# Performance work log

Measured on AMD Instinct MI355X. Metric: run time of the kernel, lower is better.

The kernel has to match this reference:

```python
import jax, jax.numpy as jnp
import numpy as np

NUM_LAYERS = 4
HIDDEN = 32
INPUT = 2
B = 16384
T = 64


def setup_inputs() -> dict:
    key = jax.random.key(0)
    ks = jax.random.split(key, 8)
    s = 1.0 / np.sqrt(HIDDEN)  # PyTorch LSTM default init scale
    return {
        "x": jax.random.normal(ks[0], (B, 3, T), dtype=jnp.float32),
        "W_ih0": jax.random.uniform(ks[1], (4 * HIDDEN, INPUT), minval=-s, maxval=s, dtype=jnp.float32),
        "W_ih": jax.random.uniform(ks[2], (NUM_LAYERS - 1, 4 * HIDDEN, HIDDEN), minval=-s, maxval=s, dtype=jnp.float32),
        "W_hh": jax.random.uniform(ks[3], (NUM_LAYERS, 4 * HIDDEN, HIDDEN), minval=-s, maxval=s, dtype=jnp.float32),
        "b_ih": jax.random.uniform(ks[4], (NUM_LAYERS, 4 * HIDDEN), minval=-s, maxval=s, dtype=jnp.float32),
        "b_hh": jax.random.uniform(ks[5], (NUM_LAYERS, 4 * HIDDEN), minval=-s, maxval=s, dtype=jnp.float32),
        "W_lin": jax.random.uniform(ks[6], (1, HIDDEN), minval=-s, maxval=s, dtype=jnp.float32),
        "b_lin": jax.random.uniform(ks[7], (1,), minval=-s, maxval=s, dtype=jnp.float32),
    }


def _lstm_cell(inp, h, c, Wih, Whh, b):
    # inp: [B, in_dim]; h, c: [B, H]; Wih: [4H, in_dim]; Whh: [4H, H]; b: [4H]
    gates = inp @ Wih.T + h @ Whh.T + b  # [B, 4H]
    i, f, g, o = jnp.split(gates, 4, axis=-1)  # PyTorch gate order: i, f, g, o
    i = jax.nn.sigmoid(i)
    f = jax.nn.sigmoid(f)
    g = jnp.tanh(g)
    o = jax.nn.sigmoid(o)
    c_new = f * c + i * g
    h_new = o * jnp.tanh(c_new)
    return h_new, c_new


def reference(x, W_ih0, W_ih, W_hh, b_ih, b_hh, W_lin, b_lin):
    # x: [B, 3, T]; channel 2 (id) is discarded, as in the original forward.
    feats = x[:, :2, :]                         # [B, 2, T]
    xs = jnp.transpose(feats, (2, 0, 1))        # [T, B, 2]
    bsz = x.shape[0]
    h0 = jnp.zeros((NUM_LAYERS, bsz, HIDDEN), dtype=x.dtype)
    c0 = jnp.zeros((NUM_LAYERS, bsz, HIDDEN), dtype=x.dtype)
    bias = b_ih + b_hh  # [L, 4H]

    def step(carry, xt):
        h, c = carry  # each [L, B, H]
        inp = xt
        hs, cs = [], []
        for l in range(NUM_LAYERS):
            Wih = W_ih0 if l == 0 else W_ih[l - 1]
            h_new, c_new = _lstm_cell(inp, h[l], c[l], Wih, W_hh[l], bias[l])
            hs.append(h_new)
            cs.append(c_new)
            inp = h_new
        return (jnp.stack(hs), jnp.stack(cs)), None

    (h, c), _ = jax.lax.scan(step, (h0, c0), xs)
    # last timestep's top-layer output -> linear -> sigmoid -> squeeze to [B]
    out = jax.nn.sigmoid(h[-1] @ W_lin.T + b_lin)  # [B, 1]
    return out.squeeze(-1)
```

## Files before the change

kernel.cpp:

```cpp
#include <hip/hip_runtime.h>

typedef float  f32x4  __attribute__((ext_vector_type(4)));
typedef short  bf16x8 __attribute__((ext_vector_type(8)));

#define LOG2E    1.4426950408889634f
#define TWOLOG2E 2.8853900817779268f

__device__ __forceinline__ unsigned short f2b(float f) {
    unsigned int u = __builtin_bit_cast(unsigned int, f);
    u += 0x7fffu + ((u >> 16) & 1u);
    return (unsigned short)(u >> 16);
}
__device__ __forceinline__ float b2f(unsigned short s) {
    unsigned int u = ((unsigned int)s) << 16;
    return __builtin_bit_cast(float, u);
}
__device__ __forceinline__ unsigned int pk2(float lo, float hi) {
    return (unsigned int)f2b(lo) | ((unsigned int)f2b(hi) << 16);
}
__device__ __forceinline__ float sig2(float xh) {
    return __builtin_amdgcn_rcpf(1.0f + __builtin_amdgcn_exp2f(-xh));
}
__device__ __forceinline__ float th2(float xh) {
    return 2.0f * __builtin_amdgcn_rcpf(1.0f + __builtin_amdgcn_exp2f(-xh)) - 1.0f;
}
__device__ __forceinline__ float thc(float c) {
    return 2.0f * __builtin_amdgcn_rcpf(1.0f + __builtin_amdgcn_exp2f(c * -TWOLOG2E)) - 1.0f;
}

__global__ __launch_bounds__(256, 4)
void lstm_mfma(const float* __restrict__ xg,  const float* __restrict__ Wih0,
               const float* __restrict__ Wih, const float* __restrict__ Whh,
               const float* __restrict__ bih, const float* __restrict__ bhh,
               const float* __restrict__ Wlin,const float* __restrict__ blin,
               float* __restrict__ out) {
    __shared__ short        hb[4 * 2 * 640] __attribute__((aligned(16)));
    __shared__ unsigned int xb[64 * 16];

    const int tid  = threadIdx.x;
    const int wv   = __builtin_amdgcn_readfirstlane(tid >> 6);
    const int lane = tid & 63;
    const int m    = lane & 15;
    const int q    = lane >> 4;
    const int row0 = blockIdx.x * 16;

    for (int i = tid; i < 2560; i += 256) ((unsigned int*)hb)[i] = 0u;

    for (int i = tid; i < 1024; i += 256) {
        int r = i >> 6, t = i & 63;
        float x0 = xg[(size_t)(row0 + r) * 192 + t];
        float x1 = xg[(size_t)(row0 + r) * 192 + 64 + t];
        xb[t * 16 + r] = pk2(x0, x1);
    }

    bf16x8 bfr[8][2];
    float  bv[8];
#pragma unroll
    for (int g = 0; g < 8; ++g) {
        const int   T    = g >> 1;
        const int   rowG = T * 32 + 2 * m + (g & 1);
        const float sc   = (T == 2) ? TWOLOG2E : LOG2E;
        bv[g] = (bih[wv * 128 + rowG] + bhh[wv * 128 + rowG]) * sc;
#pragma unroll
        for (int c = 0; c < 2; ++c) {
            const int k0 = c * 32 + q * 8;
            float w[8];
            if (wv == 0) {
                if (c == 0) {
#pragma unroll
                    for (int jj = 0; jj < 8; ++jj) w[jj] = 0.0f;
                    if (q == 0) { w[0] = Wih0[rowG * 2]; w[1] = Wih0[rowG * 2 + 1]; }
                } else {
                    const float* src = Whh + rowG * 32 + (k0 - 32);
#pragma unroll
                    for (int jj = 0; jj < 8; ++jj) w[jj] = src[jj];
                }
            } else {
                const float* src = (c == 0) ? (Wih + (wv - 1) * 4096 + rowG * 32 + k0)
                                            : (Whh + wv * 4096 + rowG * 32 + (k0 - 32));
#pragma unroll
                for (int jj = 0; jj < 8; ++jj) w[jj] = src[jj];
            }
            bf16x8 fr;
#pragma unroll
            for (int jj = 0; jj < 8; ++jj) fr[jj] = (short)f2b(w[jj] * sc);
            bfr[g][c] = fr;
        }
    }

    float cst[2][4];
#pragma unroll
    for (int hf = 0; hf < 2; ++hf)
#pragma unroll
        for (int r = 0; r < 4; ++r) cst[hf][r] = 0.0f;

    __syncthreads();

    for (int s = 0; s < 67; ++s) {
        const int t = s - wv;
        if (t >= 0 && t < 64) {
            const int rp = (s + 1) & 1;
            const int wp = s & 1;
            const short* hrin  = hb + ((wv > 0 ? wv - 1 : 0) * 2 + rp) * 640;
            const short* hrrec = hb + (wv * 2 + rp) * 640;
            short*       hw    = hb + (wv * 2 + wp) * 640;

            bf16x8 a0, a1;
            if (wv == 0) {
                unsigned int xd = xb[t * 16 + m];
                unsigned int lo = (q == 0) ? xd : 0u;
                union { unsigned int u[4]; bf16x8 v; } au;
                au.u[0] = lo; au.u[1] = 0u; au.u[2] = 0u; au.u[3] = 0u;
                a0 = au.v;
            } else {
                a0 = *(const bf16x8*)(hrin + m * 40 + q * 8);
            }
            a1 = *(const bf16x8*)(hrrec + m * 40 + q * 8);

            float h0[4];
#pragma unroll
            for (int hf = 0; hf < 2; ++hf) {
                f32x4 zz = {0.f, 0.f, 0.f, 0.f};
                f32x4 ai = __builtin_amdgcn_mfma_f32_16x16x32_bf16(a0, bfr[0 + hf][0], zz, 0, 0, 0);
                ai       = __builtin_amdgcn_mfma_f32_16x16x32_bf16(a1, bfr[0 + hf][1], ai, 0, 0, 0);
                f32x4 af = __builtin_amdgcn_mfma_f32_16x16x32_bf16(a0, bfr[2 + hf][0], zz, 0, 0, 0);
                af       = __builtin_amdgcn_mfma_f32_16x16x32_bf16(a1, bfr[2 + hf][1], af, 0, 0, 0);
                f32x4 ag = __builtin_amdgcn_mfma_f32_16x16x32_bf16(a0, bfr[4 + hf][0], zz, 0, 0, 0);
                ag       = __builtin_amdgcn_mfma_f32_16x16x32_bf16(a1, bfr[4 + hf][1], ag, 0, 0, 0);
                f32x4 ao = __builtin_amdgcn_mfma_f32_16x16x32_bf16(a0, bfr[6 + hf][0], zz, 0, 0, 0);
                ao       = __builtin_amdgcn_mfma_f32_16x16x32_bf16(a1, bfr[6 + hf][1], ao, 0, 0, 0);
#pragma unroll
                for (int r = 0; r < 4; ++r) {
                    float i_ = sig2(ai[r] + bv[0 + hf]);
                    float f_ = sig2(af[r] + bv[2 + hf]);
                    float g_ = th2 (ag[r] + bv[4 + hf]);
                    float o_ = sig2(ao[r] + bv[6 + hf]);
                    float cn = f_ * cst[hf][r] + i_ * g_;
                    cst[hf][r] = cn;
                    float hh = o_ * thc(cn);
                    if (hf == 0) {
                        h0[r] = hh;
                    } else {
                        ((unsigned int*)hw)[(q * 4 + r) * 20 + m] = pk2(h0[r], hh);
                    }
                }
            }
        }
        __syncthreads();
    }

    if (tid < 16) {
        const short* h3 = hb + (3 * 2 + 0) * 640;
        float s = blin[0];
#pragma unroll
        for (int k = 0; k < 32; ++k)
            s += Wlin[k] * b2f((unsigned short)h3[tid * 40 + k]);
        out[row0 + tid] = sig2(s * LOG2E);
    }
}

extern "C" void kernel_launch(void* const* d_in, const int* in_sizes, int n_in,
                              void* d_out, int out_size, void* d_ws, size_t ws_size,
                              hipStream_t stream) {
    const float* x    = (const float*)d_in[0];
    const float* Wih0 = (const float*)d_in[1];
    const float* Wih  = (const float*)d_in[2];
    const float* Whh  = (const float*)d_in[3];
    const float* bih  = (const float*)d_in[4];
    const float* bhh  = (const float*)d_in[5];
    const float* Wlin = (const float*)d_in[6];
    const float* blin = (const float*)d_in[7];
    float* out = (float*)d_out;

    lstm_mfma<<<1024, 256, 0, stream>>>(x, Wih0, Wih, Whh, bih, bhh, Wlin, blin, out);
}
```

Baseline: 261.7 us.

## Process two row tiles and two timesteps per sync with fused gate math

Each block now handles 32 batch rows as two 16-row tiles, and each wavefront advances two timesteps per barrier using a deeper double-buffered LDS layout, which halves the number of __syncthreads in the layer-wavefront pipeline. The bias is folded into the MFMA accumulator init and pre-negated scaling is applied to weights. The gate math is restructured to share reciprocals (sigmoid·tanh combined into one rcp). The costs are fewer blocks, higher register pressure and more LDS (launch bounds drop to 2 blocks/CU), and intra-wave dependency between the two timesteps.

```diff
diff --git a/kernel.cpp b/kernel.cpp
--- a/kernel.cpp
+++ b/kernel.cpp
@@ -3,8 +3,9 @@
 typedef float  f32x4  __attribute__((ext_vector_type(4)));
 typedef short  bf16x8 __attribute__((ext_vector_type(8)));
 
-#define LOG2E    1.4426950408889634f
-#define TWOLOG2E 2.8853900817779268f
+#define LOG2E      1.4426950408889634f
+#define NLOG2E    -1.4426950408889634f
+#define NTWOLOG2E -2.8853900817779268f
 
 __device__ __forceinline__ unsigned short f2b(float f) {
     unsigned int u = __builtin_bit_cast(unsigned int, f);
@@ -18,39 +19,32 @@
 __device__ __forceinline__ unsigned int pk2(float lo, float hi) {
     return (unsigned int)f2b(lo) | ((unsigned int)f2b(hi) << 16);
 }
-__device__ __forceinline__ float sig2(float xh) {
-    return __builtin_amdgcn_rcpf(1.0f + __builtin_amdgcn_exp2f(-xh));
-}
-__device__ __forceinline__ float th2(float xh) {
-    return 2.0f * __builtin_amdgcn_rcpf(1.0f + __builtin_amdgcn_exp2f(-xh)) - 1.0f;
-}
-__device__ __forceinline__ float thc(float c) {
-    return 2.0f * __builtin_amdgcn_rcpf(1.0f + __builtin_amdgcn_exp2f(c * -TWOLOG2E)) - 1.0f;
-}
+__device__ __forceinline__ float frcp(float x) { return __builtin_amdgcn_rcpf(x); }
+__device__ __forceinline__ float fex2(float x) { return __builtin_amdgcn_exp2f(x); }
 
-__global__ __launch_bounds__(256, 4)
+__global__ __launch_bounds__(256, 2)
 void lstm_mfma(const float* __restrict__ xg,  const float* __restrict__ Wih0,
                const float* __restrict__ Wih, const float* __restrict__ Whh,
                const float* __restrict__ bih, const float* __restrict__ bhh,
                const float* __restrict__ Wlin,const float* __restrict__ blin,
                float* __restrict__ out) {
-    __shared__ short        hb[4 * 2 * 640] __attribute__((aligned(16)));
-    __shared__ unsigned int xb[64 * 16];
+    __shared__ short        hb[16 * 1280] __attribute__((aligned(16)));
+    __shared__ unsigned int xb[64 * 32];
 
     const int tid  = threadIdx.x;
     const int wv   = __builtin_amdgcn_readfirstlane(tid >> 6);
     const int lane = tid & 63;
     const int m    = lane & 15;
     const int q    = lane >> 4;
-    const int row0 = blockIdx.x * 16;
+    const int row0 = blockIdx.x * 32;
 
-    for (int i = tid; i < 2560; i += 256) ((unsigned int*)hb)[i] = 0u;
+    for (int i = tid; i < 10240; i += 256) ((unsigned int*)hb)[i] = 0u;
 
-    for (int i = tid; i < 1024; i += 256) {
+    for (int i = tid; i < 2048; i += 256) {
         int r = i >> 6, t = i & 63;
         float x0 = xg[(size_t)(row0 + r) * 192 + t];
         float x1 = xg[(size_t)(row0 + r) * 192 + 64 + t];
-        xb[t * 16 + r] = pk2(x0, x1);
+        xb[t * 32 + r] = pk2(x0, x1);
     }
 
     bf16x8 bfr[8][2];
@@ -59,7 +53,7 @@
     for (int g = 0; g < 8; ++g) {
         const int   T    = g >> 1;
         const int   rowG = T * 32 + 2 * m + (g & 1);
-        const float sc   = (T == 2) ? TWOLOG2E : LOG2E;
+        const float sc   = (T == 2) ? NTWOLOG2E : NLOG2E;
         bv[g] = (bih[wv * 128 + rowG] + bhh[wv * 128 + rowG]) * sc;
 #pragma unroll
         for (int c = 0; c < 2; ++c) {
@@ -88,74 +82,87 @@
         }
     }
 
-    float cst[2][4];
+    float cst[2][2][4];
 #pragma unroll
-    for (int hf = 0; hf < 2; ++hf)
+    for (int tt = 0; tt < 2; ++tt)
 #pragma unroll
-        for (int r = 0; r < 4; ++r) cst[hf][r] = 0.0f;
+        for (int hf = 0; hf < 2; ++hf)
+#pragma unroll
+            for (int r = 0; r < 4; ++r) cst[tt][hf][r] = 0.0f;
 
     __syncthreads();
 
-    for (int s = 0; s < 67; ++s) {
-        const int t = s - wv;
-        if (t >= 0 && t < 64) {
-            const int rp = (s + 1) & 1;
-            const int wp = s & 1;
-            const short* hrin  = hb + ((wv > 0 ? wv - 1 : 0) * 2 + rp) * 640;
-            const short* hrrec = hb + (wv * 2 + rp) * 640;
-            short*       hw    = hb + (wv * 2 + wp) * 640;
-
+    auto cell_step = [&](int t, const short* pa0, const short* pa1, short* hwr) {
+#pragma unroll
+        for (int tt = 0; tt < 2; ++tt) {
             bf16x8 a0, a1;
             if (wv == 0) {
-                unsigned int xd = xb[t * 16 + m];
-                unsigned int lo = (q == 0) ? xd : 0u;
+                unsigned int xd = xb[t * 32 + tt * 16 + m];
                 union { unsigned int u[4]; bf16x8 v; } au;
-                au.u[0] = lo; au.u[1] = 0u; au.u[2] = 0u; au.u[3] = 0u;
+                au.u[0] = (q == 0) ? xd : 0u; au.u[1] = 0u; au.u[2] = 0u; au.u[3] = 0u;
                 a0 = au.v;
             } else {
-                a0 = *(const bf16x8*)(hrin + m * 40 + q * 8);
+                a0 = *(const bf16x8*)(pa0 + (tt * 16 + m) * 40 + q * 8);
             }
-            a1 = *(const bf16x8*)(hrrec + m * 40 + q * 8);
+            a1 = *(const bf16x8*)(pa1 + (tt * 16 + m) * 40 + q * 8);
 
+            f32x4 acc[8];
+#pragma unroll
+            for (int g = 0; g < 8; ++g) {
+                f32x4 cb = {bv[g], bv[g], bv[g], bv[g]};
+                acc[g] = __builtin_amdgcn_mfma_f32_16x16x32_bf16(a0, bfr[g][0], cb, 0, 0, 0);
+                acc[g] = __builtin_amdgcn_mfma_f32_16x16x32_bf16(a1, bfr[g][1], acc[g], 0, 0, 0);
+            }
             float h0[4];
 #pragma unroll
             for (int hf = 0; hf < 2; ++hf) {
-                f32x4 zz = {0.f, 0.f, 0.f, 0.f};
-                f32x4 ai = __builtin_amdgcn_mfma_f32_16x16x32_bf16(a0, bfr[0 + hf][0], zz, 0, 0, 0);
-                ai       = __builtin_amdgcn_mfma_f32_16x16x32_bf16(a1, bfr[0 + hf][1], ai, 0, 0, 0);
-                f32x4 af = __builtin_amdgcn_mfma_f32_16x16x32_bf16(a0, bfr[2 + hf][0], zz, 0, 0, 0);
-                af       = __builtin_amdgcn_mfma_f32_16x16x32_bf16(a1, bfr[2 + hf][1], af, 0, 0, 0);
-                f32x4 ag = __builtin_amdgcn_mfma_f32_16x16x32_bf16(a0, bfr[4 + hf][0], zz, 0, 0, 0);
-                ag       = __builtin_amdgcn_mfma_f32_16x16x32_bf16(a1, bfr[4 + hf][1], ag, 0, 0, 0);
-                f32x4 ao = __builtin_amdgcn_mfma_f32_16x16x32_bf16(a0, bfr[6 + hf][0], zz, 0, 0, 0);
-                ao       = __builtin_amdgcn_mfma_f32_16x16x32_bf16(a1, bfr[6 + hf][1], ao, 0, 0, 0);
 #pragma unroll
                 for (int r = 0; r < 4; ++r) {
-                    float i_ = sig2(ai[r] + bv[0 + hf]);
-                    float f_ = sig2(af[r] + bv[2 + hf]);
-                    float g_ = th2 (ag[r] + bv[4 + hf]);
-                    float o_ = sig2(ao[r] + bv[6 + hf]);
-                    float cn = f_ * cst[hf][r] + i_ * g_;
-                    cst[hf][r] = cn;
-                    float hh = o_ * thc(cn);
+                    float ei = fex2(acc[0 + hf][r]);
+                    float ef = fex2(acc[2 + hf][r]);
+                    float eg = fex2(acc[4 + hf][r]);
+                    float eo = fex2(acc[6 + hf][r]);
+                    float ig = (1.0f - eg) * frcp((1.0f + ei) * (1.0f + eg));
+                    float fc = cst[tt][hf][r] * frcp(1.0f + ef);
+                    float cn = ig + fc;
+                    cst[tt][hf][r] = cn;
+                    float ec = fex2(cn * NTWOLOG2E);
+                    float hh = (1.0f - ec) * frcp((1.0f + eo) * (1.0f + ec));
                     if (hf == 0) {
                         h0[r] = hh;
                     } else {
-                        ((unsigned int*)hw)[(q * 4 + r) * 20 + m] = pk2(h0[r], hh);
+                        ((unsigned int*)hwr)[(tt * 16 + q * 4 + r) * 20 + m] = pk2(h0[r], hh);
                     }
                 }
             }
         }
+    };
+
+    for (int S = 0; S < 35; ++S) {
+        const int t0 = 2 * (S - wv);
+        if (t0 >= 0 && t0 <= 62) {
+            const int p  = S & 1;
+            const int pb = p ^ 1;
+            short*       Lc0 = hb + ((wv * 2 + p ) * 2    ) * 1280;
+            short*       Lc1 = Lc0 + 1280;
+            const short* Lp1 = hb + ((wv * 2 + pb) * 2 + 1) * 1280;
+            const int    lb  = (wv > 0) ? (wv - 1) : 0;
+            const short* Dp0 = hb + ((lb * 2 + pb) * 2    ) * 1280;
+            const short* Dp1 = Dp0 + 1280;
+
+            cell_step(t0,     Dp0, Lp1, Lc0);
+            cell_step(t0 + 1, Dp1, Lc0, Lc1);
+        }
         __syncthreads();
     }
 
-    if (tid < 16) {
-        const short* h3 = hb + (3 * 2 + 0) * 640;
+    if (tid < 32) {
+        const short* h3 = hb + ((3 * 2 + 0) * 2 + 1) * 1280;
         float s = blin[0];
 #pragma unroll
         for (int k = 0; k < 32; ++k)
             s += Wlin[k] * b2f((unsigned short)h3[tid * 40 + k]);
-        out[row0 + tid] = sig2(s * LOG2E);
+        out[row0 + tid] = frcp(1.0f + fex2(s * NLOG2E));
     }
 }
 
@@ -172,5 +179,5 @@
     const float* blin = (const float*)d_in[7];
     float* out = (float*)d_out;
 
-    lstm_mfma<<<1024, 256, 0, stream>>>(x, Wih0, Wih, Whh, bih, bhh, Wlin, blin, out);
+    lstm_mfma<<<512, 256, 0, stream>>>(x, Wih0, Wih, Whh, bih, bhh, Wlin, blin, out);
 }
```

After: 232.7 us. 1.12x faster.
